# Kernel tuning notes

Hardware: AMD Instinct MI355X
Metric: run time of the kernel (lower is better)

The kernel has to match this reference:

```python
import jax, jax.numpy as jnp
import numpy as np

N_HEAD = 4
N_BIT = 8      # ssm coder bits, table_len = 2**8 = 256
IN_DIM = 8
FFN_V = 4      # ffn coder bits, 2**4 = 16 codes per head
FFN_DEPTH = 8  # tree depth, 2**8 = 256 leaves
TBL = 2 ** N_BIT


def _bern(key, logits):
    # torch.bernoulli(logits.sigmoid())
    return jax.random.uniform(key, logits.shape) < jax.nn.sigmoid(logits)


def _bool2long(x, n):
    mul = (2 ** (n - 1 - jnp.arange(n))).astype(jnp.int32)
    return (x.astype(jnp.int32) * mul).sum(-1)


def _long2bool(x, n):
    mul = (2 ** (n - 1 - jnp.arange(n))).astype(jnp.int32)
    return ((x[..., None] // mul) % 2).astype(bool)


def _tree_ffn(q, qs, key_p, val_p, rng):
    # q: (N, Q) bool, qs: (N, Q) float  (qs broadcast per head, matching intent)
    N, Q = q.shape
    H, depth = N_HEAD, FFN_DEPTH
    nv = 2 ** depth
    nk = nv - 1
    qf = jnp.broadcast_to(q[:, None, :], (N, H, Q)).reshape(N * H, Q)
    qs = jnp.broadcast_to(qs[:, None, :], (N, H, Q)).reshape(N * H, Q)
    qs = (2.0 * qf.astype(qs.dtype) - 1.0) * qs
    ix_h = jnp.arange(N * H, dtype=jnp.int32) % H
    ix = jnp.zeros(N * H, dtype=jnp.int32)
    key_flat = key_p.reshape(-1, 2 * Q)  # (H*nk, 2Q)
    support = None
    for d in range(depth):
        ix_k = ix_h * nk + (2 ** d - 1) + ix
        kw = key_flat[ix_k]  # (NH, 2Q)
        kb = _bern(jax.random.fold_in(rng, d), kw).reshape(-1, Q, 2)
        k1 = kb[:, :, 0].astype(qs.dtype)
        k2 = kb[:, :, 1].astype(qs.dtype)
        k1 = -jnp.logaddexp(-k1, qs)
        k2 = -jnp.logaddexp(-k2, -qs)
        lor_s = jnp.logaddexp(k1, k2)
        lor_s = -jax.nn.logsumexp(-lor_s, axis=-1)  # (NH,)
        lor = _bern(jax.random.fold_in(rng, 100 + d), lor_s)
        lor_s = (2.0 * lor.astype(qs.dtype) - 1.0) * lor_s
        ix = 2 * ix + lor.astype(jnp.int32)
        support = lor_s if support is None else -jnp.logaddexp(-support, -lor_s)
    vw = val_p.reshape(-1, val_p.shape[-1])[ix_h * nv + ix]  # (NH, V)
    vb = _bern(jax.random.fold_in(rng, 999), vw)
    vs = (2.0 * vb.astype(qs.dtype) - 1.0) * vw
    vs = -jnp.logaddexp(-vs, -support[:, None])
    return vb.reshape(N, H, -1), vs.reshape(N, H, -1)


def _forward(x, xs, ffn_key, ffn_value, table, state0):
    rng = jax.random.key(42)
    B, L, D = x.shape
    H, V, T = N_HEAD, FFN_V, TBL
    xb, xss = _tree_ffn(x.reshape(-1, D), xs.reshape(-1, D), ffn_key, ffn_value,
                        jax.random.fold_in(rng, 1))
    xb = xb.reshape(B, L, H, V)
    xss = xss.reshape(B, L, H, V)
    xcode = _bool2long(xb, V)                      # (B,L,H) in [0,16)
    xss = -jax.nn.logsumexp(-xss, axis=-1)         # (B,L,H)
    # sample stochastic lookup tables, independently per batch element
    tlog = jnp.broadcast_to(table, (B,) + table.shape[1:])  # (B,64,T,8)
    tb = _bern(jax.random.fold_in(rng, 2), tlog)
    table_s = table * (2.0 * tb.astype(xs.dtype) - 1.0)
    tcode = _bool2long(tb, N_BIT)                  # (B,64,T) in [0,T)
    table_s = -jax.nn.logsumexp(-table_s, axis=-1) # (B,64,T)
    head_off = (jnp.arange(L * H, dtype=jnp.int32) % H) * (2 ** V)
    idx = xcode.reshape(B, L * H) + head_off[None, :]
    y = jnp.take_along_axis(tcode, idx[:, :, None], axis=1).reshape(B, L, H, T)
    ys = jnp.take_along_axis(table_s, idx[:, :, None], axis=1).reshape(B, L, H, T)
    ys = -jnp.logaddexp(-ys, -xss[..., None])
    # Blelloch-style doubling scan; compose = table gather + soft-AND in log domain
    i = 1
    while i < L:
        y1 = y[:, :L - i]
        z = jnp.take_along_axis(y[:, i:], y1, axis=-1)
        zs = -jnp.logaddexp(-ys[:, :L - i], -jnp.take_along_axis(ys[:, i:], y1, axis=-1))
        y = jnp.concatenate([y[:, :i], z], axis=1)
        ys = jnp.concatenate([ys[:, :i], zs], axis=1)
        i *= 2
    # initial state
    s0b = _bern(jax.random.fold_in(rng, 3), jnp.broadcast_to(state0, (B,) + state0.shape[1:]))
    s0s = state0 * (2.0 * s0b.astype(xs.dtype) - 1.0)  # (B,H,8)
    s0 = _bool2long(s0b, N_BIT)                        # (B,H)
    s0s = -jax.nn.logsumexp(-s0s, axis=-1)             # (B,H)
    sidx = jnp.broadcast_to(s0[:, None, :, None], (B, L, H, 1))
    z = jnp.take_along_axis(y, sidx, axis=-1)[..., 0]   # (B,L,H)
    zs = jnp.take_along_axis(ys, sidx, axis=-1)[..., 0]
    zs = -jnp.logaddexp(-s0s[:, None, :], -zs)
    zb = _long2bool(z, N_BIT)                           # (B,L,H,8)
    zs = jnp.broadcast_to(zs[..., None], zb.shape)
    return zb.reshape(B, L, H * N_BIT), zs.reshape(B, L, H * N_BIT)


def setup_inputs() -> dict:
    key = jax.random.key(0)
    k = jax.random.split(key, 6)
    B, L = 8, 4096
    x = jax.random.randint(k[0], (B, L, IN_DIM), 0, 2).astype(bool)
    xs = jax.random.normal(k[1], (B, L, IN_DIM), dtype=jnp.float32)
    ffn_key = jax.random.normal(k[2], (N_HEAD, 2 ** FFN_DEPTH - 1, 2 * IN_DIM), dtype=jnp.float32) + 3.0
    ffn_value = jax.random.normal(k[3], (N_HEAD, 2 ** FFN_DEPTH, FFN_V), dtype=jnp.float32) + 3.0
    table = jax.random.normal(k[4], (1, (2 ** FFN_V) * N_HEAD, TBL, N_BIT), dtype=jnp.float32)
    state0 = jax.random.normal(k[5], (1, N_HEAD, N_BIT), dtype=jnp.float32)
    return {"x": x, "xs": xs, "ffn_key": ffn_key, "ffn_value": ffn_value,
            "table": table, "state0": state0}


def reference(x, xs, ffn_key, ffn_value, table, state0):
    return _forward(x, xs, ffn_key, ffn_value, table, state0)
```

## Files before the change

### kernel.cpp

```cpp
#include <hip/hip_runtime.h>
#include <stdint.h>
#include <math.h>

#define BB 8
#define LL 4096
#define HH 4
#define DD 8
#define VV 4
#define DEPTH 8
#define NBIT 8
#define NROW 131072
#define CHUNK 64
#define NCHUNK 64
#define GRID 1024
#define NLEAF 32

typedef int v4i __attribute__((ext_vector_type(4)));

__device__ __forceinline__ uint32_t rotl32(uint32_t v, int r){ return (v<<r)|(v>>(32-r)); }

__device__ __forceinline__ void tf2x32(uint32_t k0, uint32_t k1, uint32_t x0, uint32_t x1,
                                       uint32_t& o0, uint32_t& o1){
  uint32_t ks2 = k0 ^ k1 ^ 0x1BD11BDAu;
  x0 += k0; x1 += k1;
  x0+=x1; x1=rotl32(x1,13); x1^=x0;
  x0+=x1; x1=rotl32(x1,15); x1^=x0;
  x0+=x1; x1=rotl32(x1,26); x1^=x0;
  x0+=x1; x1=rotl32(x1, 6); x1^=x0;
  x0+=k1; x1+=ks2+1u;
  x0+=x1; x1=rotl32(x1,17); x1^=x0;
  x0+=x1; x1=rotl32(x1,29); x1^=x0;
  x0+=x1; x1=rotl32(x1,16); x1^=x0;
  x0+=x1; x1=rotl32(x1,24); x1^=x0;
  x0+=ks2; x1+=k0+2u;
  x0+=x1; x1=rotl32(x1,13); x1^=x0;
  x0+=x1; x1=rotl32(x1,15); x1^=x0;
  x0+=x1; x1=rotl32(x1,26); x1^=x0;
  x0+=x1; x1=rotl32(x1, 6); x1^=x0;
  x0+=k0; x1+=k1+3u;
  x0+=x1; x1=rotl32(x1,17); x1^=x0;
  x0+=x1; x1=rotl32(x1,29); x1^=x0;
  x0+=x1; x1=rotl32(x1,16); x1^=x0;
  x0+=x1; x1=rotl32(x1,24); x1^=x0;
  x0+=k1; x1+=ks2+4u;
  x0+=x1; x1=rotl32(x1,13); x1^=x0;
  x0+=x1; x1=rotl32(x1,15); x1^=x0;
  x0+=x1; x1=rotl32(x1,26); x1^=x0;
  x0+=x1; x1=rotl32(x1, 6); x1^=x0;
  x0+=ks2; x1+=k0+5u;
  o0 = x0; o1 = x1;
}

struct K2 { uint32_t a, b; };
__device__ __forceinline__ K2 kfold(K2 k, uint32_t d){
  K2 r; tf2x32(k.a, k.b, 0u, d, r.a, r.b); return r;
}

__device__ __forceinline__ uint32_t rbits(K2 k, uint32_t p){
  uint32_t o0, o1; tf2x32(k.a, k.b, 0u, p, o0, o1); return o0 ^ o1;
}

__device__ __forceinline__ float bits2u(uint32_t b){
  return __uint_as_float((b >> 9) | 0x3f800000u) - 1.0f;
}

__device__ __forceinline__ float xla_expf(float x){
  #pragma clang fp contract(off)
  const float exp_hi = 88.3762626647950f;
  const float exp_lo = -88.3762626647949f;
  const float log2e  = 1.44269504088896341f;
  const float c1 = 0.693359375f;
  const float c2 = -2.12194440e-4f;
  float xc = fmaxf(fminf(x, exp_hi), exp_lo);
  float fx = floorf(xc * log2e + 0.5f);
  float tmp = fx * c1;
  float z1  = fx * c2;
  float r = xc - tmp;
  r = r - z1;
  float z = r * r;
  float y = 1.9875691500E-4f;
  y = y * r + 1.3981999507E-3f;
  y = y * r + 8.3334519073E-3f;
  y = y * r + 4.1665795894E-2f;
  y = y * r + 1.6666665459E-1f;
  y = y * r + 5.0000001201E-1f;
  y = y * z + r;
  y = y + 1.0f;
  int emm0 = (int)fx + 127;
  float scale = __int_as_float(emm0 << 23);
  return fmaxf(y * scale, x);
}

__device__ __forceinline__ float xla_logf(float a){
  #pragma clang fp contract(off)
  float x = fmaxf(a, __uint_as_float(0x00800000u));
  uint32_t bits = __float_as_uint(x);
  int em = (int)(bits >> 23) - 126;
  x = __uint_as_float((bits & 0x007fffffu) | 0x3f000000u);
  float e = (float)em;
  bool mlt = x < 0.707106781186547524f;
  float tmp1 = mlt ? x : 0.0f;
  float xm = x - 1.0f;
  e = e - (mlt ? 1.0f : 0.0f);
  xm = xm + tmp1;
  float z = xm * xm;
  float y = 7.0376836292E-2f;
  y = y * xm + (-1.1514610310E-1f);
  y = y * xm + 1.1676998740E-1f;
  y = y * xm + (-1.2420140846E-1f);
  y = y * xm + 1.4249322787E-1f;
  y = y * xm + (-1.6668057665E-1f);
  y = y * xm + 2.0000714765E-1f;
  y = y * xm + (-2.4999993993E-1f);
  y = y * xm + 3.3333331174E-1f;
  y = y * xm;
  y = y * z;
  y = e * (-2.12194440e-4f) + y;
  y = y - 0.5f * z;
  float res = xm + y;
  res = e * 0.693359375f + res;
  return res;
}

__device__ __forceinline__ float xla_log1pf(float x){
  #pragma clang fp contract(off)
  if (fabsf(x) < 1e-4f){
    return ((-0.5f * x) + 1.0f) * x;
  }
  return xla_logf(1.0f + x);
}

__device__ __forceinline__ float xla_logaddexp(float a, float b){
  #pragma clang fp contract(off)
  float m = fmaxf(a, b);
  float d = a - b;
  return m + xla_log1pf(xla_expf(-fabsf(d)));
}

template<int NV>
__device__ __forceinline__ float neg_lse_neg(const float* v){
  #pragma clang fp contract(off)
  float m = -v[0];
  #pragma unroll
  for (int i = 1; i < NV; i++) m = fmaxf(m, -v[i]);
  float s = 0.f;
  #pragma unroll
  for (int i = 0; i < NV; i++) s = s + xla_expf((-v[i]) - m);
  return -(xla_logf(s) + m);
}

__device__ __forceinline__ float xla_sigmoid(float w){
  #pragma clang fp contract(off)
  float e = xla_expf(-w);
  return 1.0f / (1.0f + e);
}

__device__ __forceinline__ float andf(float a, float b){
  float na = -a, nb = -b;
  float m = fmaxf(na, nb);
  float d = fabsf(na - nb);
  return -(m + log1pf(expf(-d)));
}
#define AND_IDENT 1e30f

__device__ __forceinline__ void cstore_u8(uint8_t* p, uint32_t v){
  asm volatile("global_store_byte %0, %1, off sc0 sc1" :: "v"(p), "v"(v) : "memory");
}
__device__ __forceinline__ void cstore_f32(float* p, float v){
  asm volatile("global_store_dword %0, %1, off sc0 sc1" :: "v"(p), "v"(v) : "memory");
}
__device__ __forceinline__ uint32_t cload_u8(const uint8_t* p){
  uint32_t v;
  asm volatile("global_load_ubyte %0, %1, off sc0 sc1\n\ts_waitcnt vmcnt(0)"
               : "=v"(v) : "v"(p) : "memory");
  return v;
}
__device__ __forceinline__ float cload_f32(const float* p){
  float v;
  asm volatile("global_load_dword %0, %1, off sc0 sc1\n\ts_waitcnt vmcnt(0)"
               : "=v"(v) : "v"(p) : "memory");
  return v;
}
__device__ __forceinline__ uint32_t cload_u32(const uint32_t* p){
  uint32_t v;
  asm volatile("global_load_dword %0, %1, off sc0 sc1\n\ts_waitcnt vmcnt(0)"
               : "=v"(v) : "v"(p) : "memory");
  return v;
}
__device__ __forceinline__ v4i cload_b128(const v4i* p){
  v4i v;
  asm volatile("global_load_dwordx4 %0, %1, off sc0 sc1\n\ts_waitcnt vmcnt(0)"
               : "=v"(v) : "v"(p) : "memory");
  return v;
}

__device__ __forceinline__ void gbar(uint32_t* leaves, uint32_t* root, uint32_t epoch){
  __syncthreads();
  if (threadIdx.x == 0){
    uint32_t leaf = blockIdx.x & (NLEAF - 1);
    uint32_t old = atomicAdd(&leaves[leaf * 32], 1u);
    if (old + 1u == epoch * (GRID / NLEAF))
      atomicAdd(root, 1u);
    int slp = 1;
    while (cload_u32(root) < epoch * NLEAF){
      for (int i = 0; i < slp; i++) __builtin_amdgcn_s_sleep(15);
      if (slp < 4) slp <<= 1;
    }
  }
  __syncthreads();
}

__global__ __launch_bounds__(256) void k_pre(const uint32_t* xw, int* flag,
                      const float* s0w, int* s0code, float* s0s,
                      const float* fk, const float* fv,
                      float* sigFK, float* sigFV, uint32_t* keys, uint32_t* barmem){
  int i = blockIdx.x * 256 + threadIdx.x;
  if (i < 16320) sigFK[i] = xla_sigmoid(fk[i]);
  else if (i < 16320 + 4096) sigFV[i - 16320] = xla_sigmoid(fv[i - 16320]);

  if (blockIdx.x == 1){
    for (int k = threadIdx.x; k < 1025; k += 256) barmem[k] = 0u;
  }
  if (blockIdx.x == 0){
    __shared__ int any;
    int t = threadIdx.x;
    if (t == 0) any = 0;
    __syncthreads();
    int bad = 0;
    for (int k = t; k < 1024; k += 256){
      uint32_t w = xw[k];
      if (w != 0u && w != 1u && w != 0x3F800000u) bad = 1;
    }
    if (bad) atomicOr(&any, 1);
    __syncthreads();
    if (t == 0) *flag = any;

    if (t < 32){
      int b = t >> 2, h = t & 3;
      K2 root{0u, 42u};
      K2 sk = kfold(root, 3u);
      float v[NBIT];
      uint32_t code = 0;
      #pragma unroll
      for (int j = 0; j < NBIT; j++){
        float w = s0w[h*NBIT + j];
        uint32_t p = (uint32_t)((b*4 + h)*NBIT + j);
        float u = bits2u(rbits(sk, p));
        bool bit = u < xla_sigmoid(w);
        code |= (bit ? 1u : 0u) << (NBIT - 1 - j);
        v[j] = bit ? w : -w;
      }
      s0code[t] = (int)code;
      s0s[t]    = neg_lse_neg<NBIT>(v);
    }
    if (t == 0){
      K2 root{0u, 42u};
      K2 rngT = kfold(root, 1u);
      for (int d = 0; d < DEPTH; d++){
        K2 kd = kfold(rngT, (uint32_t)d);
        keys[2*d] = kd.a; keys[2*d+1] = kd.b;
        K2 lk = kfold(rngT, 100u + (uint32_t)d);
        keys[16+2*d] = lk.a; keys[16+2*d+1] = lk.b;
      }
      K2 vk = kfold(rngT, 999u);
      keys[32] = vk.a; keys[33] = vk.b;
      K2 tk = kfold(root, 2u);
      keys[34] = tk.a; keys[35] = tk.b;
    }
  }
}

__global__ __launch_bounds__(256, 4) void k_fused(
    const void* xraw, const float* xs, const float* fv,
    const float* table, float* out,
    uint8_t* xcode, float* xss, uint8_t* tcode, float* tabs,
    uint8_t* F, uint8_t* zOut, float* P, float* T,
    const int* s0code, const float* s0s, const int* flag,
    const float* sigFK, const float* sigFV, const uint32_t* keys,
    uint32_t* leaves, uint32_t* rootc){

  __shared__ v4i sT4[256];
  __shared__ v4i sF4[1024];
  __shared__ uint8_t sXC[CHUNK];
  __shared__ float carryL[4];
  uint8_t* sT = (uint8_t*)sT4;
  uint8_t* sF = (uint8_t*)sF4;
  const int blk = blockIdx.x;
  const int t = threadIdx.x;

  if (blk >= 512){
    int idx = (blk - 512) * 256 + t;
    int rem = idx & 16383;
    K2 tk{keys[34], keys[35]};
    float4 w0 = *(const float4*)(table + (size_t)rem*NBIT);
    float4 w1 = *(const float4*)(table + (size_t)rem*NBIT + 4);
    float w[NBIT] = {w0.x,w0.y,w0.z,w0.w,w1.x,w1.y,w1.z,w1.w};
    float v[NBIT];
    uint32_t code = 0;
    #pragma unroll
    for (int j = 0; j < NBIT; j++){
      float u = bits2u(rbits(tk, (uint32_t)idx * 8u + (uint32_t)j));
      bool bit = u < xla_sigmoid(w[j]);
      code |= (bit ? 1u : 0u) << (NBIT - 1 - j);
      v[j] = bit ? w[j] : -w[j];
    }
    cstore_u8(tcode + idx, code);
    cstore_f32(tabs + idx, neg_lse_neg<NBIT>(v));
  } else {
    int r = blk * 256 + t;
    int n = r >> 2;
    int h = r & 3;
    bool u8mode = (*flag != 0);
    const uint8_t* x8   = (const uint8_t*)xraw;
    const uint32_t* x32 = (const uint32_t*)xraw;

    float L0[DD], L1[DD], L2[DD], L3[DD];
    #pragma unroll
    for (int j = 0; j < DD; j++){
      bool qb = u8mode ? (x8[n*DD + j] != 0) : (x32[n*DD + j] != 0u);
      float v = xs[n*DD + j];
      float q = qb ? v : -v;
      float A0 = -xla_logaddexp(-0.0f, q);
      float A1 = -xla_logaddexp(-1.0f, q);
      float B0 = -xla_logaddexp(-0.0f, -q);
      float B1 = -xla_logaddexp(-1.0f, -q);
      L0[j] = xla_logaddexp(A0, B0);
      L1[j] = xla_logaddexp(A1, B0);
      L2[j] = xla_logaddexp(A0, B1);
      L3[j] = xla_logaddexp(A1, B1);
    }

    const float* hb = sigFK + (size_t)h * 255 * 16;
    float cur[16];
    #pragma unroll
    for (int q4 = 0; q4 < 4; q4++)
      *(float4*)(cur + 4*q4) = *(const float4*)(hb + 4*q4);

    uint32_t ix = 0;
    float support = 0.f;

    for (int d = 0; d < 7; d++){
      float cl[16], cr[16];
      {
        const float* cb = hb + (size_t)((2 << d) - 1 + 2*(int)ix) * 16;
        #pragma unroll
        for (int q4 = 0; q4 < 4; q4++){
          *(float4*)(cl + 4*q4) = *(const float4*)(cb + 4*q4);
          *(float4*)(cr + 4*q4) = *(const float4*)(cb + 16 + 4*q4);
        }
      }
      K2 kd{keys[2*d], keys[2*d+1]};
      float lor[DD];
      #pragma unroll
      for (int j = 0; j < DD; j++){
        uint32_t p1 = (uint32_t)r * 16u + 2u*(uint32_t)j;
        float u1 = bits2u(rbits(kd, p1));
        float u2 = bits2u(rbits(kd, p1 + 1u));
        bool b1 = u1 < cur[2*j];
        bool b2 = u2 < cur[2*j + 1];
        float t01 = b1 ? L1[j] : L0[j];
        float t23 = b1 ? L3[j] : L2[j];
        lor[j] = b2 ? t23 : t01;
      }
      float lor_s = neg_lse_neg<DD>(lor);
      K2 lk{keys[16+2*d], keys[16+2*d+1]};
      float ul = bits2u(rbits(lk, (uint32_t)r));
      bool lb = ul < xla_sigmoid(lor_s);
      float ls = lb ? lor_s : -lor_s;
      ix = 2u*ix + (lb ? 1u : 0u);
      support = (d == 0) ? ls : -xla_logaddexp(-support, -ls);
      #pragma unroll
      for (int q = 0; q < 16; q++) cur[q] = lb ? cr[q] : cl[q];
    }

    float fvv[8], sfv[8];
    {
      const float* fb = fv    + (size_t)(h*256 + 2*(int)ix) * VV;
      const float* sb = sigFV + (size_t)(h*256 + 2*(int)ix) * VV;
      *(float4*)(fvv)     = *(const float4*)(fb);
      *(float4*)(fvv + 4) = *(const float4*)(fb + 4);
      *(float4*)(sfv)     = *(const float4*)(sb);
      *(float4*)(sfv + 4) = *(const float4*)(sb + 4);
    }
    {
      const int d = 7;
      K2 kd{keys[2*d], keys[2*d+1]};
      float lor[DD];
      #pragma unroll
      for (int j = 0; j < DD; j++){
        uint32_t p1 = (uint32_t)r * 16u + 2u*(uint32_t)j;
        float u1 = bits2u(rbits(kd, p1));
        float u2 = bits2u(rbits(kd, p1 + 1u));
        bool b1 = u1 < cur[2*j];
        bool b2 = u2 < cur[2*j + 1];
        float t01 = b1 ? L1[j] : L0[j];
        float t23 = b1 ? L3[j] : L2[j];
        lor[j] = b2 ? t23 : t01;
      }
      float lor_s = neg_lse_neg<DD>(lor);
      K2 lk{keys[16+2*d], keys[16+2*d+1]};
      float ul = bits2u(rbits(lk, (uint32_t)r));
      bool lb = ul < xla_sigmoid(lor_s);
      float ls = lb ? lor_s : -lor_s;
      support = -xla_logaddexp(-support, -ls);
      #pragma unroll
      for (int c = 0; c < VV; c++){
        fvv[c] = lb ? fvv[4+c] : fvv[c];
        sfv[c] = lb ? sfv[4+c] : sfv[c];
      }
    }

    K2 vk{keys[32], keys[33]};
    float vs[VV];
    uint32_t code = 0;
    #pragma unroll
    for (int c = 0; c < VV; c++){
      float u = bits2u(rbits(vk, (uint32_t)r*4u + (uint32_t)c));
      bool b = u < sfv[c];
      code |= (b ? 1u : 0u) << (VV - 1 - c);
      float sv = b ? fvv[c] : -fvv[c];
      vs[c] = -xla_logaddexp(-sv, -support);
    }
    cstore_u8(xcode + r, code);
    cstore_f32(xss + r, neg_lse_neg<VV>(vs));
  }
  gbar(leaves, rootc, 1u);

  for (int v = blk; v < 2048; v += 1024){
    int c  = v & 63;
    int bh = v >> 6;
    int b = bh >> 2, h = bh & 3;
    const int rowbase = (b*64 + h*16) * 256;
    sT4[t] = cload_b128((const v4i*)(tcode + rowbase) + t);
    if (t < CHUNK){
      sXC[t] = (uint8_t)cload_u8(xcode + (b*LL + c*CHUNK + t)*HH + h);
    }
    __syncthreads();
    int cur = t;
    #pragma unroll 8
    for (int k = 0; k < CHUNK; k++){
      cur = sT[(int)sXC[k]*256 + cur];
    }
    cstore_u8(F + (size_t)v*256 + t, (uint32_t)cur);
    __syncthreads();
  }
  gbar(leaves, rootc, 2u);

  if (blk < 512){
    int bh = blk >> 4;
    int b = bh >> 2, h = bh & 3;
    int w = t >> 6, lane = t & 63;
    int c = (blk & 15)*4 + w;
    const int rowbase = (b*64 + h*16) * 256;
    sT4[t] = cload_b128((const v4i*)(tcode + rowbase) + t);
    const v4i* Fb4 = (const v4i*)(F + (size_t)bh * 16384);
    #pragma unroll
    for (int i = 0; i < 4; i++) sF4[t + 256*i] = cload_b128(Fb4 + t + 256*i);

    int l = c*CHUNK + lane;
    int r = (b*LL + l)*HH + h;
    int   xcv = (int)cload_u8(xcode + r);
    float xsv = cload_f32(xss + r);
    __syncthreads();

    int z = s0code[bh];
    for (int k = 0; k < c; k++) z = sF[k*256 + z];

    int aReg = 0, zReg = 0;
    for (int k = 0; k < CHUNK; k++){
      int xck = __shfl(xcv, k, 64);
      int a = xck*256 + z;
      z = sT[a];
      if (lane == k){ aReg = a; zReg = z; }
    }

    float p = andf(cload_f32(tabs + rowbase + aReg), xsv);
    #pragma unroll
    for (int off = 1; off < 64; off <<= 1){
      float o = __shfl_up(p, off, 64);
      if (lane >= off) p = andf(o, p);
    }
    int vblk = bh*64 + c;
    cstore_u8(zOut + vblk*CHUNK + lane, (uint32_t)zReg);
    cstore_f32(P + vblk*CHUNK + lane, p);
    if (lane == 63) cstore_f32(T + vblk, p);
  }
  gbar(leaves, rootc, 3u);

  if (blk < 512){
    int c = blk & 63;
    int b = blk >> 6;
    int w = t >> 6, lane = t & 63;

    float val = (lane < c) ? cload_f32(T + (b*4 + w)*64 + lane) : AND_IDENT;
    #pragma unroll
    for (int off = 1; off < 64; off <<= 1){
      float o = __shfl_xor(val, off, 64);
      val = andf(val, o);
    }
    float carry = andf(val, s0s[b*4 + w]);
    if (lane == 0) carryL[w] = carry;
    __syncthreads();

    int k = t >> 2, h = t & 3;
    int cblk = (b*4 + h)*64 + c;
    int z = (int)cload_u8(zOut + cblk*CHUNK + k);
    float sc = andf(carryL[h], cload_f32(P + cblk*CHUNK + k));

    size_t base = (size_t)blk*2048 + (size_t)t*8;
    float4 b0, b1;
    b0.x = (float)((z >> 7) & 1); b0.y = (float)((z >> 6) & 1);
    b0.z = (float)((z >> 5) & 1); b0.w = (float)((z >> 4) & 1);
    b1.x = (float)((z >> 3) & 1); b1.y = (float)((z >> 2) & 1);
    b1.z = (float)((z >> 1) & 1); b1.w = (float)( z       & 1);
    float4 s4; s4.x = sc; s4.y = sc; s4.z = sc; s4.w = sc;
    *(float4*)(out + base)     = b0;
    *(float4*)(out + base + 4) = b1;
    *(float4*)(out + 1048576 + base)     = s4;
    *(float4*)(out + 1048576 + base + 4) = s4;
  }
}

extern "C" void kernel_launch(void* const* d_in, const int* in_sizes, int n_in,
                              void* d_out, int out_size, void* d_ws, size_t ws_size,
                              hipStream_t stream) {
  const void*  x      = d_in[0];
  const float* xs     = (const float*)d_in[1];
  const float* fk     = (const float*)d_in[2];
  const float* fv     = (const float*)d_in[3];
  const float* table  = (const float*)d_in[4];
  const float* s0w    = (const float*)d_in[5];
  float* out          = (float*)d_out;

  uint8_t* ws = (uint8_t*)d_ws;
  uint8_t* xcode_ = ws;
  uint8_t* tcode_ = ws + 131072;
  uint8_t* F_     = ws + 262144;
  float*   xss_   = (float*)(ws + 786432);
  float*   tabs_  = (float*)(ws + 1310720);
  uint8_t* zOut_  = ws + 1835008;
  float*   P_     = (float*)(ws + 1966080);
  float*   T_     = (float*)(ws + 2490368);
  int*     s0code_= (int*)  (ws + 2498560);
  float*   s0s_   = (float*)(ws + 2498688);
  int*     flag_  = (int*)  (ws + 2498816);
  float*   sigFK_ = (float*)(ws + 2499072);
  float*   sigFV_ = (float*)(ws + 2564352);
  uint32_t* keys_ = (uint32_t*)(ws + 2580736);
  uint32_t* barmem_=(uint32_t*)(ws + 2581504);
  uint32_t* leaves_= barmem_;
  uint32_t* rootc_ = barmem_ + 1024;

  k_pre  <<<82, 256, 0, stream>>>((const uint32_t*)x, flag_, s0w, s0code_, s0s_,
                                  fk, fv, sigFK_, sigFV_, keys_, barmem_);
  k_fused<<<GRID, 256, 0, stream>>>(x, xs, fv, table, out,
                                    xcode_, xss_, tcode_, tabs_,
                                    F_, zOut_, P_, T_,
                                    s0code_, s0s_, flag_, sigFK_, sigFV_, keys_,
                                    leaves_, rootc_);
}
```

Measured before the change: 167.9 us.

## Split tree-FFN walk across thread pairs and fold table coding into odd lanes

The tree-FFN descent for each (row, head) is now split over two adjacent threads. Each thread handles four of the eight input dimensions, and the per-level terms are exchanged with wavefront shuffles. The table-coding work that used to run in separate blocks is folded into the odd threads after the tree walk, so every block does both kinds of work. The aim is to balance load across all 1024 blocks and halve the serial per-thread dependency chain and register footprint. In exchange it adds shuffles, duplicates the RNG and sigmoid work in both partners, and makes the table coding run after the walk on the same threads.

After: 183.9 us. +9.5%, slower.

```diff
diff --git a/kernel.cpp b/kernel.cpp
--- a/kernel.cpp
+++ b/kernel.cpp
@@ -288,35 +288,22 @@
   const int blk = blockIdx.x;
   const int t = threadIdx.x;
 
-  if (blk >= 512){
-    int idx = (blk - 512) * 256 + t;
-    int rem = idx & 16383;
-    K2 tk{keys[34], keys[35]};
-    float4 w0 = *(const float4*)(table + (size_t)rem*NBIT);
-    float4 w1 = *(const float4*)(table + (size_t)rem*NBIT + 4);
-    float w[NBIT] = {w0.x,w0.y,w0.z,w0.w,w1.x,w1.y,w1.z,w1.w};
-    float v[NBIT];
-    uint32_t code = 0;
-    #pragma unroll
-    for (int j = 0; j < NBIT; j++){
-      float u = bits2u(rbits(tk, (uint32_t)idx * 8u + (uint32_t)j));
-      bool bit = u < xla_sigmoid(w[j]);
-      code |= (bit ? 1u : 0u) << (NBIT - 1 - j);
-      v[j] = bit ? w[j] : -w[j];
-    }
-    cstore_u8(tcode + idx, code);
-    cstore_f32(tabs + idx, neg_lse_neg<NBIT>(v));
-  } else {
-    int r = blk * 256 + t;
+  {
+    int g = blk * 256 + t;
+    int lane = t & 63;
+    bool isA = (t & 1) == 0;
+    int r = g >> 1;
     int n = r >> 2;
     int h = r & 3;
+    int jb = isA ? 0 : 4;
     bool u8mode = (*flag != 0);
     const uint8_t* x8   = (const uint8_t*)xraw;
     const uint32_t* x32 = (const uint32_t*)xraw;
 
-    float L0[DD], L1[DD], L2[DD], L3[DD];
+    float L0[4], L1[4], L2[4], L3[4];
     #pragma unroll
-    for (int j = 0; j < DD; j++){
+    for (int jj = 0; jj < 4; jj++){
+      int j = jb + jj;
       bool qb = u8mode ? (x8[n*DD + j] != 0) : (x32[n*DD + j] != 0u);
       float v = xs[n*DD + j];
       float q = qb ? v : -v;
@@ -324,43 +311,48 @@
       float A1 = -xla_logaddexp(-1.0f, q);
       float B0 = -xla_logaddexp(-0.0f, -q);
       float B1 = -xla_logaddexp(-1.0f, -q);
-      L0[j] = xla_logaddexp(A0, B0);
-      L1[j] = xla_logaddexp(A1, B0);
-      L2[j] = xla_logaddexp(A0, B1);
-      L3[j] = xla_logaddexp(A1, B1);
-    }
-
-    const float* hb = sigFK + (size_t)h * 255 * 16;
-    float cur[16];
-    #pragma unroll
-    for (int q4 = 0; q4 < 4; q4++)
-      *(float4*)(cur + 4*q4) = *(const float4*)(hb + 4*q4);
+      L0[jj] = xla_logaddexp(A0, B0);
+      L1[jj] = xla_logaddexp(A1, B0);
+      L2[jj] = xla_logaddexp(A0, B1);
+      L3[jj] = xla_logaddexp(A1, B1);
+    }
+
+    const float* hbase = sigFK + (size_t)h * 255 * 16;
+    float cur[8];
+    *(float4*)(cur)     = *(const float4*)(hbase + jb*2);
+    *(float4*)(cur + 4) = *(const float4*)(hbase + jb*2 + 4);
 
     uint32_t ix = 0;
     float support = 0.f;
 
     for (int d = 0; d < 7; d++){
-      float cl[16], cr[16];
+      float cl[8], cr[8];
       {
-        const float* cb = hb + (size_t)((2 << d) - 1 + 2*(int)ix) * 16;
-        #pragma unroll
-        for (int q4 = 0; q4 < 4; q4++){
-          *(float4*)(cl + 4*q4) = *(const float4*)(cb + 4*q4);
-          *(float4*)(cr + 4*q4) = *(const float4*)(cb + 16 + 4*q4);
-        }
+        const float* cb = hbase + (size_t)((2 << d) - 1 + 2*(int)ix) * 16 + jb*2;
+        *(float4*)(cl)     = *(const float4*)(cb);
+        *(float4*)(cl + 4) = *(const float4*)(cb + 4);
+        *(float4*)(cr)     = *(const float4*)(cb + 16);
+        *(float4*)(cr + 4) = *(const float4*)(cb + 20);
       }
       K2 kd{keys[2*d], keys[2*d+1]};
-      float lor[DD];
-      #pragma unroll
-      for (int j = 0; j < DD; j++){
+      float myl[4];
+      #pragma unroll
+      for (int jj = 0; jj < 4; jj++){
+        int j = jb + jj;
         uint32_t p1 = (uint32_t)r * 16u + 2u*(uint32_t)j;
         float u1 = bits2u(rbits(kd, p1));
         float u2 = bits2u(rbits(kd, p1 + 1u));
-        bool b1 = u1 < cur[2*j];
-        bool b2 = u2 < cur[2*j + 1];
-        float t01 = b1 ? L1[j] : L0[j];
-        float t23 = b1 ? L3[j] : L2[j];
-        lor[j] = b2 ? t23 : t01;
+        bool b1 = u1 < cur[2*jj];
+        bool b2 = u2 < cur[2*jj + 1];
+        float t01 = b1 ? L1[jj] : L0[jj];
+        float t23 = b1 ? L3[jj] : L2[jj];
+        myl[jj] = b2 ? t23 : t01;
+      }
+      float lor[8];
+      #pragma unroll
+      for (int i = 0; i < 4; i++){
+        lor[i]     = __shfl(myl[i], lane & 62, 64);
+        lor[4 + i] = __shfl(myl[i], lane | 1, 64);
       }
       float lor_s = neg_lse_neg<DD>(lor);
       K2 lk{keys[16+2*d], keys[16+2*d+1]};
@@ -370,7 +362,7 @@
       ix = 2u*ix + (lb ? 1u : 0u);
       support = (d == 0) ? ls : -xla_logaddexp(-support, -ls);
       #pragma unroll
-      for (int q = 0; q < 16; q++) cur[q] = lb ? cr[q] : cl[q];
+      for (int q = 0; q < 8; q++) cur[q] = lb ? cr[q] : cl[q];
     }
 
     float fvv[8], sfv[8];
@@ -385,17 +377,24 @@
     {
       const int d = 7;
       K2 kd{keys[2*d], keys[2*d+1]};
-      float lor[DD];
-      #pragma unroll
-      for (int j = 0; j < DD; j++){
+      float myl[4];
+      #pragma unroll
+      for (int jj = 0; jj < 4; jj++){
+        int j = jb + jj;
         uint32_t p1 = (uint32_t)r * 16u + 2u*(uint32_t)j;
         float u1 = bits2u(rbits(kd, p1));
         float u2 = bits2u(rbits(kd, p1 + 1u));
-        bool b1 = u1 < cur[2*j];
-        bool b2 = u2 < cur[2*j + 1];
-        float t01 = b1 ? L1[j] : L0[j];
-        float t23 = b1 ? L3[j] : L2[j];
-        lor[j] = b2 ? t23 : t01;
+        bool b1 = u1 < cur[2*jj];
+        bool b2 = u2 < cur[2*jj + 1];
+        float t01 = b1 ? L1[jj] : L0[jj];
+        float t23 = b1 ? L3[jj] : L2[jj];
+        myl[jj] = b2 ? t23 : t01;
+      }
+      float lor[8];
+      #pragma unroll
+      for (int i = 0; i < 4; i++){
+        lor[i]     = __shfl(myl[i], lane & 62, 64);
+        lor[4 + i] = __shfl(myl[i], lane | 1, 64);
       }
       float lor_s = neg_lse_neg<DD>(lor);
       K2 lk{keys[16+2*d], keys[16+2*d+1]};
@@ -421,8 +420,30 @@
       float sv = b ? fvv[c] : -fvv[c];
       vs[c] = -xla_logaddexp(-sv, -support);
     }
-    cstore_u8(xcode + r, code);
-    cstore_f32(xss + r, neg_lse_neg<VV>(vs));
+    if (isA){
+      cstore_u8(xcode + r, code);
+      cstore_f32(xss + r, neg_lse_neg<VV>(vs));
+    }
+
+    if (!isA){
+      int idx = r;
+      int rem = idx & 16383;
+      K2 tk{keys[34], keys[35]};
+      float4 w0 = *(const float4*)(table + (size_t)rem*NBIT);
+      float4 w1 = *(const float4*)(table + (size_t)rem*NBIT + 4);
+      float w[NBIT] = {w0.x,w0.y,w0.z,w0.w,w1.x,w1.y,w1.z,w1.w};
+      float v[NBIT];
+      uint32_t tc = 0;
+      #pragma unroll
+      for (int j = 0; j < NBIT; j++){
+        float u = bits2u(rbits(tk, (uint32_t)idx * 8u + (uint32_t)j));
+        bool bit = u < xla_sigmoid(w[j]);
+        tc |= (bit ? 1u : 0u) << (NBIT - 1 - j);
+        v[j] = bit ? w[j] : -w[j];
+      }
+      cstore_u8(tcode + idx, tc);
+      cstore_f32(tabs + idx, neg_lse_neg<NBIT>(v));
+    }
   }
   gbar(leaves, rootc, 1u);
 
```

## Fold chunk-transition composition into tree phase and drop a grid barrier

Applied to the files above, without the earlier changes.

Tree-walk blocks now keep their computed codes in shared memory. They wait on a counter that the table-sampling blocks increment when done, then compose the chunk transition maps for all four heads directly, removing one full grid barrier and a separate phase. The tree loop is also unrolled, with the next depth's random numbers generated ahead to overlap with the current step. The spin-wait adds a cross-block dependency and possible stalls, and the composition work now sits on 512 blocks with 4 heads each rather than spread across 1024.

Result: no change. 165.9 us (-1.2%).

```diff
diff --git a/kernel.cpp b/kernel.cpp
--- a/kernel.cpp
+++ b/kernel.cpp
@@ -219,7 +219,7 @@
   else if (i < 16320 + 4096) sigFV[i - 16320] = xla_sigmoid(fv[i - 16320]);
 
   if (blockIdx.x == 1){
-    for (int k = threadIdx.x; k < 1025; k += 256) barmem[k] = 0u;
+    for (int k = threadIdx.x; k < 1040; k += 256) barmem[k] = 0u;
   }
   if (blockIdx.x == 0){
     __shared__ int any;
@@ -277,11 +277,11 @@
     uint8_t* F, uint8_t* zOut, float* P, float* T,
     const int* s0code, const float* s0s, const int* flag,
     const float* sigFK, const float* sigFV, const uint32_t* keys,
-    uint32_t* leaves, uint32_t* rootc){
+    uint32_t* leaves, uint32_t* rootc, uint32_t* tdone){
 
   __shared__ v4i sT4[256];
   __shared__ v4i sF4[1024];
-  __shared__ uint8_t sXC[CHUNK];
+  __shared__ uint8_t sXCf[256];
   __shared__ float carryL[4];
   uint8_t* sT = (uint8_t*)sT4;
   uint8_t* sF = (uint8_t*)sF4;
@@ -306,6 +306,8 @@
     }
     cstore_u8(tcode + idx, code);
     cstore_f32(tabs + idx, neg_lse_neg<NBIT>(v));
+    __syncthreads();
+    if (t == 0) atomicAdd(tdone, 1u);
   } else {
     int r = blk * 256 + t;
     int n = r >> 2;
@@ -338,75 +340,77 @@
 
     uint32_t ix = 0;
     float support = 0.f;
-
-    for (int d = 0; d < 7; d++){
+    float fvv[8], sfv[8];
+
+    float u1a[DD], u2a[DD], ulc;
+    {
+      K2 kd{keys[0], keys[1]};
+      #pragma unroll
+      for (int j = 0; j < DD; j++){
+        uint32_t p1 = (uint32_t)r * 16u + 2u*(uint32_t)j;
+        u1a[j] = bits2u(rbits(kd, p1));
+        u2a[j] = bits2u(rbits(kd, p1 + 1u));
+      }
+      K2 lk{keys[16], keys[17]};
+      ulc = bits2u(rbits(lk, (uint32_t)r));
+    }
+
+    #pragma unroll
+    for (int d = 0; d < 8; d++){
       float cl[16], cr[16];
-      {
+      if (d < 7){
         const float* cb = hb + (size_t)((2 << d) - 1 + 2*(int)ix) * 16;
         #pragma unroll
         for (int q4 = 0; q4 < 4; q4++){
           *(float4*)(cl + 4*q4) = *(const float4*)(cb + 4*q4);
           *(float4*)(cr + 4*q4) = *(const float4*)(cb + 16 + 4*q4);
         }
-      }
-      K2 kd{keys[2*d], keys[2*d+1]};
+      } else {
+        const float* fb = fv    + (size_t)(h*256 + 2*(int)ix) * VV;
+        const float* sb = sigFV + (size_t)(h*256 + 2*(int)ix) * VV;
+        *(float4*)(fvv)     = *(const float4*)(fb);
+        *(float4*)(fvv + 4) = *(const float4*)(fb + 4);
+        *(float4*)(sfv)     = *(const float4*)(sb);
+        *(float4*)(sfv + 4) = *(const float4*)(sb + 4);
+      }
       float lor[DD];
       #pragma unroll
       for (int j = 0; j < DD; j++){
-        uint32_t p1 = (uint32_t)r * 16u + 2u*(uint32_t)j;
-        float u1 = bits2u(rbits(kd, p1));
-        float u2 = bits2u(rbits(kd, p1 + 1u));
-        bool b1 = u1 < cur[2*j];
-        bool b2 = u2 < cur[2*j + 1];
+        bool b1 = u1a[j] < cur[2*j];
+        bool b2 = u2a[j] < cur[2*j + 1];
         float t01 = b1 ? L1[j] : L0[j];
         float t23 = b1 ? L3[j] : L2[j];
         lor[j] = b2 ? t23 : t01;
       }
+      float u1n[DD], u2n[DD], uln = 0.f;
+      if (d < 7){
+        K2 kd{keys[2*(d+1)], keys[2*(d+1)+1]};
+        #pragma unroll
+        for (int j = 0; j < DD; j++){
+          uint32_t p1 = (uint32_t)r * 16u + 2u*(uint32_t)j;
+          u1n[j] = bits2u(rbits(kd, p1));
+          u2n[j] = bits2u(rbits(kd, p1 + 1u));
+        }
+        K2 lk{keys[16+2*(d+1)], keys[16+2*(d+1)+1]};
+        uln = bits2u(rbits(lk, (uint32_t)r));
+      }
       float lor_s = neg_lse_neg<DD>(lor);
-      K2 lk{keys[16+2*d], keys[16+2*d+1]};
-      float ul = bits2u(rbits(lk, (uint32_t)r));
-      bool lb = ul < xla_sigmoid(lor_s);
+      bool lb = ulc < xla_sigmoid(lor_s);
       float ls = lb ? lor_s : -lor_s;
       ix = 2u*ix + (lb ? 1u : 0u);
       support = (d == 0) ? ls : -xla_logaddexp(-support, -ls);
-      #pragma unroll
-      for (int q = 0; q < 16; q++) cur[q] = lb ? cr[q] : cl[q];
-    }
-
-    float fvv[8], sfv[8];
-    {
-      const float* fb = fv    + (size_t)(h*256 + 2*(int)ix) * VV;
-      const float* sb = sigFV + (size_t)(h*256 + 2*(int)ix) * VV;
-      *(float4*)(fvv)     = *(const float4*)(fb);
-      *(float4*)(fvv + 4) = *(const float4*)(fb + 4);
-      *(float4*)(sfv)     = *(const float4*)(sb);
-      *(float4*)(sfv + 4) = *(const float4*)(sb + 4);
-    }
-    {
-      const int d = 7;
-      K2 kd{keys[2*d], keys[2*d+1]};
-      float lor[DD];
-      #pragma unroll
-      for (int j = 0; j < DD; j++){
-        uint32_t p1 = (uint32_t)r * 16u + 2u*(uint32_t)j;
-        float u1 = bits2u(rbits(kd, p1));
-        float u2 = bits2u(rbits(kd, p1 + 1u));
-        bool b1 = u1 < cur[2*j];
-        bool b2 = u2 < cur[2*j + 1];
-        float t01 = b1 ? L1[j] : L0[j];
-        float t23 = b1 ? L3[j] : L2[j];
-        lor[j] = b2 ? t23 : t01;
-      }
-      float lor_s = neg_lse_neg<DD>(lor);
-      K2 lk{keys[16+2*d], keys[16+2*d+1]};
-      float ul = bits2u(rbits(lk, (uint32_t)r));
-      bool lb = ul < xla_sigmoid(lor_s);
-      float ls = lb ? lor_s : -lor_s;
-      support = -xla_logaddexp(-support, -ls);
-      #pragma unroll
-      for (int c = 0; c < VV; c++){
-        fvv[c] = lb ? fvv[4+c] : fvv[c];
-        sfv[c] = lb ? sfv[4+c] : sfv[c];
+      if (d < 7){
+        #pragma unroll
+        for (int q = 0; q < 16; q++) cur[q] = lb ? cr[q] : cl[q];
+        #pragma unroll
+        for (int j = 0; j < DD; j++){ u1a[j] = u1n[j]; u2a[j] = u2n[j]; }
+        ulc = uln;
+      } else {
+        #pragma unroll
+        for (int c = 0; c < VV; c++){
+          fvv[c] = lb ? fvv[4+c] : fvv[c];
+          sfv[c] = lb ? sfv[4+c] : sfv[c];
+        }
       }
     }
 
@@ -423,28 +427,37 @@
     }
     cstore_u8(xcode + r, code);
     cstore_f32(xss + r, neg_lse_neg<VV>(vs));
+    sXCf[h*64 + (t >> 2)] = (uint8_t)code;
+
+    __syncthreads();
+    if (t == 0){
+      int slp = 1;
+      while (cload_u32(tdone) < 512u){
+        for (int i = 0; i < slp; i++) __builtin_amdgcn_s_sleep(15);
+        if (slp < 4) slp <<= 1;
+      }
+    }
+    __syncthreads();
+    int b = blk >> 6, c = blk & 63;
+    #pragma unroll
+    for (int i = 0; i < 4; i++)
+      sF4[i*256 + t] = cload_b128((const v4i*)(tcode + (size_t)(b*64 + i*16)*256) + t);
+    __syncthreads();
+    int c0 = t, c1 = t, c2 = t, c3 = t;
+    for (int k = 0; k < CHUNK; k++){
+      int x0 = sXCf[k],       x1 = sXCf[64 + k];
+      int x2 = sXCf[128 + k], x3 = sXCf[192 + k];
+      c0 = sF[        x0*256 + c0];
+      c1 = sF[ 4096 + x1*256 + c1];
+      c2 = sF[ 8192 + x2*256 + c2];
+      c3 = sF[12288 + x3*256 + c3];
+    }
+    cstore_u8(F + (size_t)((b*4 + 0)*64 + c)*256 + t, (uint32_t)c0);
+    cstore_u8(F + (size_t)((b*4 + 1)*64 + c)*256 + t, (uint32_t)c1);
+    cstore_u8(F + (size_t)((b*4 + 2)*64 + c)*256 + t, (uint32_t)c2);
+    cstore_u8(F + (size_t)((b*4 + 3)*64 + c)*256 + t, (uint32_t)c3);
   }
   gbar(leaves, rootc, 1u);
-
-  for (int v = blk; v < 2048; v += 1024){
-    int c  = v & 63;
-    int bh = v >> 6;
-    int b = bh >> 2, h = bh & 3;
-    const int rowbase = (b*64 + h*16) * 256;
-    sT4[t] = cload_b128((const v4i*)(tcode + rowbase) + t);
-    if (t < CHUNK){
-      sXC[t] = (uint8_t)cload_u8(xcode + (b*LL + c*CHUNK + t)*HH + h);
-    }
-    __syncthreads();
-    int cur = t;
-    #pragma unroll 8
-    for (int k = 0; k < CHUNK; k++){
-      cur = sT[(int)sXC[k]*256 + cur];
-    }
-    cstore_u8(F + (size_t)v*256 + t, (uint32_t)cur);
-    __syncthreads();
-  }
-  gbar(leaves, rootc, 2u);
 
   if (blk < 512){
     int bh = blk >> 4;
@@ -485,7 +498,7 @@
     cstore_f32(P + vblk*CHUNK + lane, p);
     if (lane == 63) cstore_f32(T + vblk, p);
   }
-  gbar(leaves, rootc, 3u);
+  gbar(leaves, rootc, 2u);
 
   if (blk < 512){
     int c = blk & 63;
@@ -550,6 +563,7 @@
   uint32_t* barmem_=(uint32_t*)(ws + 2581504);
   uint32_t* leaves_= barmem_;
   uint32_t* rootc_ = barmem_ + 1024;
+  uint32_t* tdone_ = barmem_ + 1025;
 
   k_pre  <<<82, 256, 0, stream>>>((const uint32_t*)x, flag_, s0w, s0code_, s0s_,
                                   fk, fv, sigFK_, sigFV_, keys_, barmem_);
@@ -557,5 +571,5 @@
                                     xcode_, xss_, tcode_, tabs_,
                                     F_, zOut_, P_, T_,
                                     s0code_, s0s_, flag_, sigFK_, sigFV_, keys_,
-                                    leaves_, rootc_);
-}
+                                    leaves_, rootc_, tdone_);
+}
```
